# Optimization experiments

Hardware: AMD Instinct MI355X
Metric: run time of the kernel (lower is better)

The kernel has to match this reference:

```python
import jax, jax.numpy as jnp
import numpy as np

FEAT_STRIDE = 16
SCALES = (4, 8, 16, 32)
RATIOS = (0.5, 1.0, 2.0)
A = len(SCALES) * len(RATIOS)  # 12 anchors per location
PRE_NMS = 6000
POST_NMS = 300
NMS_THRESH = 0.7
MIN_SIZE = 16.0
B, C_IN, HF, WF = 4, 768, 64, 64


def _generate_anchors():
    base = np.array([0.0, 0.0, 15.0, 15.0])

    def whctrs(a):
        w = a[2] - a[0] + 1.0
        h = a[3] - a[1] + 1.0
        return w, h, a[0] + 0.5 * (w - 1.0), a[1] + 0.5 * (h - 1.0)

    def mk(ws, hs, xc, yc):
        ws = np.asarray(ws, dtype=np.float64)[:, None]
        hs = np.asarray(hs, dtype=np.float64)[:, None]
        return np.hstack([xc - 0.5 * (ws - 1), yc - 0.5 * (hs - 1),
                          xc + 0.5 * (ws - 1), yc + 0.5 * (hs - 1)])

    w, h, xc, yc = whctrs(base)
    size = w * h
    ratios = np.array(RATIOS)
    ws = np.round(np.sqrt(size / ratios))
    hs = np.round(ws * ratios)
    ratio_anchors = mk(ws, hs, xc, yc)
    scales = np.array(SCALES, dtype=np.float64)
    out = []
    for i in range(ratio_anchors.shape[0]):
        w, h, xc, yc = whctrs(ratio_anchors[i])
        out.append(mk(w * scales, h * scales, xc, yc))
    return np.vstack(out).astype(np.float32)  # (A, 4)


def _all_anchors(hf, wf):
    an = _generate_anchors()
    sx = np.arange(wf) * FEAT_STRIDE
    sy = np.arange(hf) * FEAT_STRIDE
    sx, sy = np.meshgrid(sx, sy)
    shifts = np.stack([sx.ravel(), sy.ravel(), sx.ravel(), sy.ravel()], axis=1).astype(np.float32)
    # shift-major, anchor-minor: (K, A, 4) -> (K*A, 4) matches bbox_pred layout
    return jnp.asarray((shifts[:, None, :] + an[None, :, :]).reshape(-1, 4))


def _conv(x, w, b):
    y = jax.lax.conv_general_dilated(x, w, (1, 1), 'SAME',
                                     dimension_numbers=('NCHW', 'OIHW', 'NCHW'))
    return y + b[None, :, None, None]


def _decode(anchors, deltas):
    w = anchors[:, 2] - anchors[:, 0] + 1.0
    h = anchors[:, 3] - anchors[:, 1] + 1.0
    cx = anchors[:, 0] + 0.5 * w
    cy = anchors[:, 1] + 0.5 * h
    dx, dy, dw, dh = deltas[:, 0], deltas[:, 1], deltas[:, 2], deltas[:, 3]
    pcx = dx * w + cx
    pcy = dy * h + cy
    pw = jnp.exp(dw) * w
    ph = jnp.exp(dh) * h
    return jnp.stack([pcx - 0.5 * pw, pcy - 0.5 * ph,
                      pcx + 0.5 * pw, pcy + 0.5 * ph], axis=1)


def _nms_keep(boxes, thresh):
    # greedy NMS on score-sorted boxes; returns boolean keep mask
    boxes = jax.lax.stop_gradient(boxes)
    n = boxes.shape[0]
    x1, y1, x2, y2 = boxes[:, 0], boxes[:, 1], boxes[:, 2], boxes[:, 3]
    areas = (x2 - x1 + 1.0) * (y2 - y1 + 1.0)
    idx = jnp.arange(n)

    def body(keep, i):
        xx1 = jnp.maximum(x1[i], x1)
        yy1 = jnp.maximum(y1[i], y1)
        xx2 = jnp.minimum(x2[i], x2)
        yy2 = jnp.minimum(y2[i], y2)
        inter = jnp.maximum(xx2 - xx1 + 1.0, 0.0) * jnp.maximum(yy2 - yy1 + 1.0, 0.0)
        iou = inter / (areas[i] + areas - inter)
        suppress = (iou > thresh) & (idx > i) & keep[i]
        return keep & ~suppress, None

    keep, _ = jax.lax.scan(body, jnp.ones(n, dtype=bool), jnp.arange(n))
    return keep


def _proposal_single(scores, deltas, anchors, im_info):
    # scores: (N,), deltas: (N,4), im_info: (3,) = [h, w, scale]
    boxes = _decode(anchors, deltas)
    x1 = jnp.clip(boxes[:, 0], 0.0, im_info[1] - 1.0)
    y1 = jnp.clip(boxes[:, 1], 0.0, im_info[0] - 1.0)
    x2 = jnp.clip(boxes[:, 2], 0.0, im_info[1] - 1.0)
    y2 = jnp.clip(boxes[:, 3], 0.0, im_info[0] - 1.0)
    boxes = jnp.stack([x1, y1, x2, y2], axis=1)
    ms = MIN_SIZE * im_info[2]
    valid = ((x2 - x1 + 1.0) >= ms) & ((y2 - y1 + 1.0) >= ms)
    scores = jnp.where(valid, scores, -jnp.inf)
    _, top_idx = jax.lax.top_k(scores, PRE_NMS)
    boxes = boxes[top_idx]
    keep = _nms_keep(boxes, NMS_THRESH)
    # first POST_NMS kept indices (boxes already score-sorted); zero-pad shortfall
    sel = jnp.sort(jnp.where(keep, jnp.arange(PRE_NMS), PRE_NMS))[:POST_NMS]
    pad = sel == PRE_NMS
    sel = jnp.minimum(sel, PRE_NMS - 1)
    return boxes[sel] * (~pad)[:, None].astype(boxes.dtype)


def setup_inputs() -> dict:
    key = jax.random.key(0)
    ks = jax.random.split(key, 4)
    features = jax.random.normal(ks[0], (B, C_IN, HF, WF), dtype=jnp.float32)
    im_info = jnp.tile(jnp.array([[1024.0, 1024.0, 1.0]], dtype=jnp.float32), (B, 1))
    W1 = jax.random.normal(ks[1], (512, C_IN, 3, 3), dtype=jnp.float32) * (2.0 / (C_IN * 9)) ** 0.5
    b1 = jnp.zeros((512,), dtype=jnp.float32)
    Ws = jax.random.normal(ks[2], (2 * A, 512, 1, 1), dtype=jnp.float32) * 0.01
    bs = jnp.zeros((2 * A,), dtype=jnp.float32)
    Wb = jax.random.normal(ks[3], (4 * A, 512, 1, 1), dtype=jnp.float32) * 0.01
    bb = jnp.zeros((4 * A,), dtype=jnp.float32)
    return {"features": features, "im_info": im_info, "W1": W1, "b1": b1,
            "Ws": Ws, "bs": bs, "Wb": Wb, "bb": bb}


def reference(features, im_info, W1, b1, Ws, bs, Wb, bb):
    # RPN head: 3x3 conv + relu, then 1x1 score/bbox heads
    x = jax.nn.relu(_conv(features, W1, b1))
    cls = _conv(x, Ws, bs)       # (B, 2A, H, W)
    bbox = _conv(x, Wb, bb)      # (B, 4A, H, W)
    b, _, hf, wf = cls.shape
    # view(B, 2, -1, W) softmax over class dim, view back -> channels [0:A]=bg, [A:2A]=fg
    prob = jax.nn.softmax(cls.reshape(b, 2, -1, wf), axis=1).reshape(cls.shape)
    fg = prob[:, A:, :, :]
    scores = fg.transpose(0, 2, 3, 1).reshape(b, -1)          # (B, H*W*A)
    deltas = bbox.transpose(0, 2, 3, 1).reshape(b, -1, 4)     # (B, H*W*A, 4)
    anchors = _all_anchors(hf, wf)
    boxes = jax.vmap(lambda s, d, ii: _proposal_single(s, d, anchors, ii))(scores, deltas, im_info)
    batch_idx = jnp.repeat(jnp.arange(b, dtype=boxes.dtype), POST_NMS)[:, None]
    rois = jnp.concatenate([batch_idx, boxes.reshape(-1, 4)], axis=1)  # (B*POST_NMS, 5)
    return rois
```

## Files before the change

kernel.cpp:

```cpp
#include <hip/hip_runtime.h>
#include <stdint.h>

#define CIN 768
#define CMID 512
#define NPIX 4096
#define NANCH 49152
#define NBATCH 4
#define PRE_NMS_N 6000
#define POST_NMS_N 300

__global__ void zeroK(uint32_t* __restrict__ p, int nWords){
  int i = blockIdx.x * 256 + threadIdx.x;
  if (i < nWords) p[i] = 0u;
}

__global__ __launch_bounds__(256) void conv3x3K(
    const float* __restrict__ feat, const float* __restrict__ W1,
    const float* __restrict__ b1, float* __restrict__ xout){
  __shared__ float wLds[9216];
  __shared__ float fLds[960];
  const int tid = threadIdx.x;
  const int g  = tid >> 3;
  const int py = tid & 7;
  const int ty0 = (blockIdx.x >> 3) << 3;
  const int tx0 = (blockIdx.x & 7) << 3;
  const int ocb = blockIdx.y << 7;
  const int b = blockIdx.z;

  const int oc_t  = tid >> 1;
  const int halfw = tid & 1;
  const float* wsrc0 = W1 + (size_t)(ocb + oc_t)*6912 + halfw*36;
  const int gq   = (oc_t>>2)*12 + (oc_t&3)*3;
  const int icl0 = halfw << 2;

  int fdst[4]; int fsrc[4]; bool fgo[4]; bool fact[4];
#pragma unroll
  for (int i=0;i<4;i++){
    int lin = tid + (i<<8);
    fact[i] = lin < 800;
    int l2 = fact[i] ? lin : 0;
    int ic = l2/100; int r2 = l2 - ic*100;
    int row = r2/10; int col = r2 - row*10;
    int gy = ty0 + row - 1, gx = tx0 + col - 1;
    fgo[i]  = fact[i] && gy>=0 && gy<64 && gx>=0 && gx<64;
    fdst[i] = ic*120 + row*12 + col;
    fsrc[i] = (ic<<12) + (gy<<6) + gx;
  }
  const float* fbase = feat + ((size_t)(b*CIN) << 12);

  float macc[4][8];
  float cacc[4][8];
#pragma unroll
  for (int q=0;q<4;q++)
#pragma unroll
    for (int j=0;j<8;j++){ macc[q][j]=0.0f; cacc[q][j]=0.0f; }

  for (int icb = 0; icb < CIN; icb += 8){
    {
      const float* s = wsrc0 + (size_t)icb*9;
      float w0[36];
#pragma unroll
      for (int m=0;m<9;m++){
        float4 v = *reinterpret_cast<const float4*>(s + (m<<2));
        w0[4*m+0]=v.x; w0[4*m+1]=v.y; w0[4*m+2]=v.z; w0[4*m+3]=v.w;
      }
#pragma unroll
      for (int r=0;r<4;r++)
#pragma unroll
        for (int k=0;k<9;k++)
          wLds[(icl0+r)*1152 + (k/3)*384 + gq + (k%3)] = w0[r*9+k];
    }
#pragma unroll
    for (int i=0;i<4;i++){
      if (fact[i]){
        float v = 0.0f;
        if (fgo[i]) v = fbase[((size_t)icb << 12) + fsrc[i]];
        fLds[fdst[i]] = v;
      }
    }
    __syncthreads();
#pragma unroll
    for (int ic=0; ic<8; ic++){
      const float* fb = &fLds[ic*120 + py*12];
      const float* wb = &wLds[ic*1152 + g*12];
#pragma unroll
      for (int ky=0;ky<3;ky++){
        float4 a = *reinterpret_cast<const float4*>(fb + ky*12);
        float4 c = *reinterpret_cast<const float4*>(fb + ky*12 + 4);
        float2 e = *reinterpret_cast<const float2*>(fb + ky*12 + 8);
        const float f[10] = {a.x,a.y,a.z,a.w,c.x,c.y,c.z,c.w,e.x,e.y};
        const float* wp = wb + ky*384;
        float4 wa = *reinterpret_cast<const float4*>(wp);
        float4 wv = *reinterpret_cast<const float4*>(wp+4);
        float4 wc = *reinterpret_cast<const float4*>(wp+8);
        const float w12[12] = {wa.x,wa.y,wa.z,wa.w, wv.x,wv.y,wv.z,wv.w,
                               wc.x,wc.y,wc.z,wc.w};
#pragma unroll
        for (int q=0;q<4;q++)
#pragma unroll
          for (int kx=0;kx<3;kx++){
            float we = w12[q*3+kx];
#pragma unroll
            for (int j=0;j<8;j++)
              cacc[q][j] = fmaf(we, f[j+kx], cacc[q][j]);
          }
      }
      if ((ic & 3) == 3){
#pragma unroll
        for (int q=0;q<4;q++)
#pragma unroll
          for (int j=0;j<8;j++){
            macc[q][j] = __fadd_rn(macc[q][j], cacc[q][j]);
            cacc[q][j] = 0.0f;
          }
      }
    }
    __syncthreads();
  }
#pragma unroll
  for (int q=0;q<4;q++){
    float bias = b1[ocb + (g<<2) + q];
    float4 o0, o1;
    float* p0 = (float*)&o0; float* p1 = (float*)&o1;
#pragma unroll
    for (int j=0;j<4;j++){
      p0[j] = fmaxf(__fadd_rn(macc[q][j],   bias), 0.0f);
      p1[j] = fmaxf(__fadd_rn(macc[q][j+4], bias), 0.0f);
    }
    size_t base = ((size_t)(b*CMID + ocb + (g<<2) + q) << 12) + ((ty0+py) << 6) + tx0;
    *reinterpret_cast<float4*>(&xout[base])     = o0;
    *reinterpret_cast<float4*>(&xout[base + 4]) = o1;
  }
}

__global__ __launch_bounds__(256) void conv1x1K(
    const float* __restrict__ x,
    const float* __restrict__ Ws, const float* __restrict__ bs,
    const float* __restrict__ Wb, const float* __restrict__ bb,
    float* __restrict__ clsRaw, float* __restrict__ bboxRaw){
  __shared__ float wLds[32*72];
  const int tid = threadIdx.x;
  const int px = tid & 63;
  const int og = tid >> 6;
  const int px0 = (blockIdx.x & 63) << 6;
  const int b = blockIdx.x >> 6;
  double m[18];
  float cc[18];
#pragma unroll
  for (int j=0;j<18;j++){ m[j]=0.0; cc[j]=0.0f; }
  for (int cb=0; cb<CMID; cb+=32){
#pragma unroll
    for (int i=0;i<9;i++){
      int lin = tid + i*256;
      int c = lin / 72;
      int j = lin - c*72;
      wLds[lin] = (j < 24) ? Ws[(size_t)j*512 + cb + c]
                           : Wb[(size_t)(j-24)*512 + cb + c];
    }
    __syncthreads();
    for (int c=0;c<32;c++){
      float xv = x[((size_t)(b*CMID + cb + c) << 12) + px0 + px];
      const float* wp = &wLds[c*72 + og*18];
#pragma unroll
      for (int j=0;j<18;j++) cc[j] = fmaf(wp[j], xv, cc[j]);
    }
#pragma unroll
    for (int j=0;j<18;j++){ m[j] += (double)cc[j]; cc[j]=0.0f; }
    __syncthreads();
  }
#pragma unroll
  for (int j=0;j<18;j++){
    int jg = og*18 + j;
    float bias = (jg < 24) ? bs[jg] : bb[jg-24];
    float v = __fadd_rn((float)m[j], bias);
    if (jg < 24) clsRaw[((size_t)(b*24 + jg) << 12) + px0 + px] = v;
    else         bboxRaw[((size_t)(b*48 + jg - 24) << 12) + px0 + px] = v;
  }
}

__global__ void decodeK(const float* __restrict__ clsRaw,
                        const float* __restrict__ bboxRaw,
                        const float* __restrict__ imInfo,
                        float* __restrict__ boxes, uint32_t* __restrict__ ubits,
                        uint32_t* __restrict__ hist1){
  int n = blockIdx.x*256 + threadIdx.x;
  if (n >= NBATCH*NANCH) return;
  int b = n / NANCH;
  int r = n - b*NANCH;
  int px = r / 12;
  int a = r - px*12;
  int yi = px >> 6, xi = px & 63;
  const int w0t[3] = {23,16,11};
  const int h0t[3] = {12,16,22};
  int ridx = a >> 2;
  int sh = 2 + (a & 3);
  float W = (float)(w0t[ridx] << sh);
  float H = (float)(h0t[ridx] << sh);
  float cx = (float)((xi << 4) + 8);
  float cy = (float)((yi << 4) + 8);

  size_t cbase = ((size_t)b*24 << 12) + px;
  float sc0 = clsRaw[cbase + ((size_t)a       << 12)];
  float sc1 = clsRaw[cbase + ((size_t)(12+a)  << 12)];
  size_t bbase = ((size_t)b*48 << 12) + px;
  float dx = bboxRaw[bbase + ((size_t)(4*a+0) << 12)];
  float dy = bboxRaw[bbase + ((size_t)(4*a+1) << 12)];
  float dw = bboxRaw[bbase + ((size_t)(4*a+2) << 12)];
  float dh = bboxRaw[bbase + ((size_t)(4*a+3) << 12)];

  float imh = imInfo[b*3+0], imw = imInfo[b*3+1], iscale = imInfo[b*3+2];

  float pcx = __fadd_rn(__fmul_rn(dx, W), cx);
  float pcy = __fadd_rn(__fmul_rn(dy, H), cy);
  float pw  = __fmul_rn(expf(dw), W);
  float ph  = __fmul_rn(expf(dh), H);
  float hw = __fmul_rn(0.5f, pw), hh = __fmul_rn(0.5f, ph);
  float x1 = __fsub_rn(pcx, hw), x2 = __fadd_rn(pcx, hw);
  float y1 = __fsub_rn(pcy, hh), y2 = __fadd_rn(pcy, hh);
  float xmax = __fsub_rn(imw, 1.0f), ymax = __fsub_rn(imh, 1.0f);
  x1 = fminf(fmaxf(x1, 0.0f), xmax);
  y1 = fminf(fmaxf(y1, 0.0f), ymax);
  x2 = fminf(fmaxf(x2, 0.0f), xmax);
  y2 = fminf(fmaxf(y2, 0.0f), ymax);
  float ms = __fmul_rn(16.0f, iscale);
  bool valid = (__fadd_rn(__fsub_rn(x2,x1),1.0f) >= ms) &&
               (__fadd_rn(__fsub_rn(y2,y1),1.0f) >= ms);

  float mm = fmaxf(sc0, sc1);
  float e0 = expf(__fsub_rn(sc0, mm));
  float e1 = expf(__fsub_rn(sc1, mm));
  float s  = __fdiv_rn(e1, __fadd_rn(e0, e1));

  uint32_t u = __float_as_uint(s);
  u = (u & 0x80000000u) ? ~u : (u | 0x80000000u);
  if (!valid) u = 0x007FFFFFu;

  float4 bx = make_float4(x1, y1, x2, y2);
  *reinterpret_cast<float4*>(&boxes[(size_t)n*4]) = bx;
  ubits[n] = u;
  atomicAdd(&hist1[((size_t)b << 16) + (u >> 16)], 1u);
}

__global__ void histLoK(const uint32_t* __restrict__ ubits,
                        const uint32_t* __restrict__ thrWS, uint32_t* __restrict__ hist2){
  int n = blockIdx.x*256 + threadIdx.x;
  if (n >= NBATCH*NANCH) return;
  int b = n / NANCH;
  uint32_t u = ubits[n];
  if ((u >> 16) == thrWS[b*4+0])
    atomicAdd(&hist2[((size_t)b << 16) + (u & 0xFFFFu)], 1u);
}

__global__ __launch_bounds__(1024) void selectK(const uint32_t* __restrict__ hist,
                                                uint32_t* __restrict__ thrWS, int stage){
  __shared__ uint32_t sA[1024];
  const int b = blockIdx.x;
  const uint32_t* h = hist + ((size_t)b << 16);
  const int tid = threadIdx.x;
  uint32_t base = (stage == 0) ? 0u : thrWS[b*4+1];
  uint32_t seg = 0;
  int b0 = tid << 6;
  for (int k=0;k<64;k++) seg += h[b0+k];
  sA[tid] = seg;
  __syncthreads();
  for (int off=1; off<1024; off<<=1){
    uint32_t v = (tid+off < 1024) ? sA[tid+off] : 0u;
    __syncthreads();
    sA[tid] += v;
    __syncthreads();
  }
  uint32_t inc = sA[tid];
  uint32_t above = inc - seg;
  if (base + above < 6000u && base + inc >= 6000u){
    uint32_t c = base + above;
    for (int bin = b0+63; bin >= b0; bin--){
      uint32_t hh = h[bin];
      if (c + hh >= 6000u){
        if (stage == 0){ thrWS[b*4+0] = (uint32_t)bin; thrWS[b*4+1] = c; }
        else { thrWS[b*4+2] = (thrWS[b*4+0] << 16) | (uint32_t)bin; thrWS[b*4+3] = c; }
        break;
      }
      c += hh;
    }
  }
}

__global__ void compactK(const uint32_t* __restrict__ ubits,
                         const uint32_t* __restrict__ thrWS,
                         uint32_t* __restrict__ cnts,
                         uint64_t* __restrict__ keyHi, uint64_t* __restrict__ keyEq){
  int n = blockIdx.x*256 + threadIdx.x;
  if (n >= NBATCH*NANCH) return;
  int b = n / NANCH;
  int r = n - b*NANCH;
  uint32_t u = ubits[n];
  uint32_t us = thrWS[b*4+2];
  if (u < us) return;
  uint64_t key = ((uint64_t)(~u) << 32) | (uint32_t)r;
  if (u > us){
    uint32_t p = atomicAdd(&cnts[b*2+0], 1u);
    if (p < 8192u) keyHi[((size_t)b << 13) + p] = key;
  } else {
    uint32_t p = atomicAdd(&cnts[b*2+1], 1u);
    if (p < 8192u) keyEq[((size_t)b << 13) + p] = key;
  }
}

__global__ __launch_bounds__(1024) void sortGatherK(
    const uint64_t* __restrict__ keyHi, const uint64_t* __restrict__ keyEq,
    const uint32_t* __restrict__ cnts, const float* __restrict__ boxes,
    float* __restrict__ rbox){
  __shared__ uint64_t keys[8192];
  const int b = blockIdx.x;
  const int tid = threadIdx.x;
  uint32_t nHi = cnts[b*2+0];
  if (nHi > 8192u) nHi = 8192u;
  uint32_t nEq = cnts[b*2+1];
  if (nEq > 8192u - nHi) nEq = 8192u - nHi;
  for (int i=tid; i<8192; i+=1024){
    uint64_t k;
    if (i < (int)nHi) k = keyHi[((size_t)b << 13) + i];
    else if (i < (int)(nHi + nEq)) k = keyEq[((size_t)b << 13) + (i - nHi)];
    else k = ~0ULL;
    keys[i] = k;
  }
  __syncthreads();
  for (unsigned kk = 2; kk <= 8192; kk <<= 1){
    for (unsigned j = kk >> 1; j > 0; j >>= 1){
      for (unsigned i = tid; i < 8192; i += 1024){
        unsigned l = i ^ j;
        if (l > i){
          bool up = ((i & kk) == 0);
          uint64_t a = keys[i], c = keys[l];
          if ((a > c) == up){ keys[i] = c; keys[l] = a; }
        }
      }
      __syncthreads();
    }
  }
  for (int r = tid; r < PRE_NMS_N; r += 1024){
    uint32_t idx = (uint32_t)(keys[r] & 0xFFFFFFFFu);
    float4 v = *reinterpret_cast<const float4*>(&boxes[((size_t)b*NANCH + idx)*4]);
    *reinterpret_cast<float4*>(&rbox[((size_t)b*PRE_NMS_N + r)*4]) = v;
  }
}

__global__ __launch_bounds__(64) void nmsMaskK(const float* __restrict__ rbox,
                                               uint64_t* __restrict__ mask){
  const int b = blockIdx.z;
  const int ib = blockIdx.y;
  const int jb = blockIdx.x;
  const int lane = threadIdx.x;
  uint64_t* mrow = &mask[(size_t)b*PRE_NMS_N*96];
  if (jb < ib){
    int ig = (ib << 6) + lane;
    if (ig < PRE_NMS_N) mrow[(size_t)ig*96 + jb] = 0ull;
    return;
  }
  __shared__ float rb[64][4];
  const int ig0 = ib << 6;
  {
    int ig = ig0 + lane;
    float4 v = make_float4(0.f,0.f,0.f,0.f);
    if (ig < PRE_NMS_N) v = *reinterpret_cast<const float4*>(&rbox[((size_t)b*PRE_NMS_N + ig)*4]);
    rb[lane][0]=v.x; rb[lane][1]=v.y; rb[lane][2]=v.z; rb[lane][3]=v.w;
  }
  const int jg = (jb << 6) + lane;
  const bool jok = jg < PRE_NMS_N;
  float4 cb = make_float4(0.f,0.f,0.f,0.f);
  if (jok) cb = *reinterpret_cast<const float4*>(&rbox[((size_t)b*PRE_NMS_N + jg)*4]);
  float areaJ = __fmul_rn(__fadd_rn(__fsub_rn(cb.z,cb.x),1.0f),
                          __fadd_rn(__fsub_rn(cb.w,cb.y),1.0f));
  __syncthreads();
#pragma unroll 4
  for (int i=0;i<64;i++){
    int ig = ig0 + i;
    if (ig >= PRE_NMS_N) break;
    float x1=rb[i][0], y1=rb[i][1], x2=rb[i][2], y2=rb[i][3];
    float areaI = __fmul_rn(__fadd_rn(__fsub_rn(x2,x1),1.0f),
                            __fadd_rn(__fsub_rn(y2,y1),1.0f));
    float xx1 = fmaxf(x1, cb.x);
    float yy1 = fmaxf(y1, cb.y);
    float xx2 = fminf(x2, cb.z);
    float yy2 = fminf(y2, cb.w);
    float ww = fmaxf(__fadd_rn(__fsub_rn(xx2,xx1),1.0f), 0.0f);
    float hh = fmaxf(__fadd_rn(__fsub_rn(yy2,yy1),1.0f), 0.0f);
    float inter = __fmul_rn(ww,hh);
    float iou = __fdiv_rn(inter, __fsub_rn(__fadd_rn(areaI, areaJ), inter));
    bool bit = jok && (jg > ig) && (iou > 0.7f);
    uint64_t wword = __ballot(bit);
    if (lane == 0) mrow[(size_t)ig*96 + jb] = wword;
  }
}

__global__ __launch_bounds__(64) void nmsScanK(const float* __restrict__ rbox,
                                               const uint64_t* __restrict__ mask,
                                               float* __restrict__ out){
  const int b = blockIdx.x;
  const int lane = threadIdx.x;
  const uint64_t* mrow = &mask[(size_t)b*PRE_NMS_N*96];
  uint64_t s0 = 0ull, s1 = 0ull;
  int cnt = 0;
  for (int i=0; i<PRE_NMS_N; i++){
    int w = i >> 6;
    uint64_t sw = (w < 64) ? __shfl(s0, w) : __shfl(s1, w-64);
    if (!((sw >> (i & 63)) & 1ull)){
      if (lane == 0){
        const float* s = &rbox[((size_t)b*PRE_NMS_N + i)*4];
        float* o = &out[(size_t)(b*POST_NMS_N + cnt)*5];
        o[0] = (float)b; o[1]=s[0]; o[2]=s[1]; o[3]=s[2]; o[4]=s[3];
      }
      cnt++;
      if (cnt == POST_NMS_N) break;
      const uint64_t* mr = mrow + (size_t)i*96;
      s0 |= mr[lane];
      if (lane < 30) s1 |= mr[64+lane];
    }
  }
  for (int r = cnt + lane; r < POST_NMS_N; r += 64){
    float* o = &out[(size_t)(b*POST_NMS_N + r)*5];
    o[0] = (float)b; o[1]=0.f; o[2]=0.f; o[3]=0.f; o[4]=0.f;
  }
}

extern "C" void kernel_launch(void* const* d_in, const int* in_sizes, int n_in,
                              void* d_out, int out_size, void* d_ws, size_t ws_size,
                              hipStream_t stream) {
  const float* features = (const float*)d_in[0];
  const float* im_info  = (const float*)d_in[1];
  const float* W1 = (const float*)d_in[2];
  const float* b1 = (const float*)d_in[3];
  const float* Ws = (const float*)d_in[4];
  const float* bs = (const float*)d_in[5];
  const float* Wb = (const float*)d_in[6];
  const float* bb = (const float*)d_in[7];
  float* out = (float*)d_out;
  char* ws = (char*)d_ws;

  const size_t offX     = 0;
  const size_t offCls   = offX     + (size_t)4*512*4096*4;
  const size_t offBbox  = offCls   + (size_t)4*24*4096*4;
  const size_t offBoxes = offBbox  + (size_t)4*48*4096*4;
  const size_t offU     = offBoxes + (size_t)4*49152*4*4;
  const size_t offH1    = offU     + (size_t)4*49152*4;
  const size_t offH2    = offH1    + (size_t)4*65536*4;
  const size_t offCtr   = offH2    + (size_t)4*65536*4;
  const size_t offKHi   = offCtr   + 256;
  const size_t offKEq   = offKHi   + (size_t)4*8192*8;
  const size_t offRbox  = offKEq   + (size_t)4*8192*8;

  float*    x       = (float*)(ws + offX);
  float*    clsRaw  = (float*)(ws + offCls);
  float*    bboxRaw = (float*)(ws + offBbox);
  float*    boxes   = (float*)(ws + offBoxes);
  uint32_t* ubits   = (uint32_t*)(ws + offU);
  uint32_t* hist1   = (uint32_t*)(ws + offH1);
  uint32_t* hist2   = (uint32_t*)(ws + offH2);
  uint32_t* thrWS   = (uint32_t*)(ws + offCtr);
  uint32_t* cnts    = thrWS + 16;
  uint64_t* keyHi   = (uint64_t*)(ws + offKHi);
  uint64_t* keyEq   = (uint64_t*)(ws + offKEq);
  float*    rbox    = (float*)(ws + offRbox);
  uint64_t* mask    = (uint64_t*)(ws + offX);

  {
    int nWords = (int)(((offCtr + 256) - offH1) / 4);
    int grid = (nWords + 255) / 256;
    zeroK<<<grid, 256, 0, stream>>>((uint32_t*)(ws + offH1), nWords);
  }
  conv3x3K<<<dim3(64, 4, 4), 256, 0, stream>>>(features, W1, b1, x);
  conv1x1K<<<256, 256, 0, stream>>>(x, Ws, bs, Wb, bb, clsRaw, bboxRaw);
  {
    int grid = (NBATCH*NANCH + 255) / 256;
    decodeK<<<grid, 256, 0, stream>>>(clsRaw, bboxRaw, im_info, boxes, ubits, hist1);
    selectK<<<4, 1024, 0, stream>>>(hist1, thrWS, 0);
    histLoK<<<grid, 256, 0, stream>>>(ubits, thrWS, hist2);
    selectK<<<4, 1024, 0, stream>>>(hist2, thrWS, 1);
    compactK<<<grid, 256, 0, stream>>>(ubits, thrWS, cnts, keyHi, keyEq);
  }
  sortGatherK<<<4, 1024, 0, stream>>>(keyHi, keyEq, cnts, boxes, rbox);
  nmsMaskK<<<dim3(94, 94, 4), 64, 0, stream>>>(rbox, mask);
  nmsScanK<<<4, 64, 0, stream>>>(rbox, mask, out);
}
```

Measured before the change: 2.498 ms.

## Widen conv3x3 tile to 8x16 pixels and use packed FP32 FMA

The 3x3 conv tile grows from 8x8 to 8x16 output pixels per block, which halves the grid and doubles each thread's work to 16 pixels times 4 output channels. Weights staged in LDS are now reused across twice as many pixels. The inner accumulation uses two-wide float vectors so the compiler can emit packed FMA instructions, which process two FP32 values per instruction on CDNA3/4. The cost is higher register pressure and a larger LDS feature tile, with only 512 blocks left for occupancy.

```diff
diff --git a/kernel.cpp b/kernel.cpp
--- a/kernel.cpp
+++ b/kernel.cpp
@@ -9,6 +9,20 @@
 #define PRE_NMS_N 6000
 #define POST_NMS_N 300
 
+typedef float v2f __attribute__((ext_vector_type(2)));
+
+#if defined(__has_builtin)
+#if __has_builtin(__builtin_elementwise_fma)
+#define PKFMA(a,b,c) __builtin_elementwise_fma(a,b,c)
+#endif
+#endif
+#ifndef PKFMA
+static __device__ inline v2f pkfma_fallback(v2f a, v2f b, v2f c){
+  v2f r; r.x = fmaf(a.x,b.x,c.x); r.y = fmaf(a.y,b.y,c.y); return r;
+}
+#define PKFMA(a,b,c) pkfma_fallback(a,b,c)
+#endif
+
 __global__ void zeroK(uint32_t* __restrict__ p, int nWords){
   int i = blockIdx.x * 256 + threadIdx.x;
   if (i < nWords) p[i] = 0u;
@@ -18,12 +32,12 @@
     const float* __restrict__ feat, const float* __restrict__ W1,
     const float* __restrict__ b1, float* __restrict__ xout){
   __shared__ float wLds[9216];
-  __shared__ float fLds[960];
+  __shared__ float fLds[4864];
   const int tid = threadIdx.x;
   const int g  = tid >> 3;
   const int py = tid & 7;
-  const int ty0 = (blockIdx.x >> 3) << 3;
-  const int tx0 = (blockIdx.x & 7) << 3;
+  const int ty0 = (blockIdx.x >> 2) << 3;
+  const int tx0 = (blockIdx.x & 3) << 4;
   const int ocb = blockIdx.y << 7;
   const int b = blockIdx.z;
 
@@ -33,27 +47,27 @@
   const int gq   = (oc_t>>2)*12 + (oc_t&3)*3;
   const int icl0 = halfw << 2;
 
-  int fdst[4]; int fsrc[4]; bool fgo[4]; bool fact[4];
-#pragma unroll
-  for (int i=0;i<4;i++){
+  int fdst[6]; int fsrc[6]; bool fgo[6]; bool fact[6];
+#pragma unroll
+  for (int i=0;i<6;i++){
     int lin = tid + (i<<8);
-    fact[i] = lin < 800;
+    fact[i] = lin < 1440;
     int l2 = fact[i] ? lin : 0;
-    int ic = l2/100; int r2 = l2 - ic*100;
-    int row = r2/10; int col = r2 - row*10;
+    int ic = l2/180; int r2 = l2 - ic*180;
+    int row = r2/18; int col = r2 - row*18;
     int gy = ty0 + row - 1, gx = tx0 + col - 1;
     fgo[i]  = fact[i] && gy>=0 && gy<64 && gx>=0 && gx<64;
-    fdst[i] = ic*120 + row*12 + col;
+    fdst[i] = ic*200 + row*20 + col;
     fsrc[i] = (ic<<12) + (gy<<6) + gx;
   }
   const float* fbase = feat + ((size_t)(b*CIN) << 12);
 
-  float macc[4][8];
-  float cacc[4][8];
+  v2f macc[4][8];
+  v2f cacc[4][8];
 #pragma unroll
   for (int q=0;q<4;q++)
 #pragma unroll
-    for (int j=0;j<8;j++){ macc[q][j]=0.0f; cacc[q][j]=0.0f; }
+    for (int j2=0;j2<8;j2++){ macc[q][j2] = (v2f){0.f,0.f}; cacc[q][j2] = (v2f){0.f,0.f}; }
 
   for (int icb = 0; icb < CIN; icb += 8){
     {
@@ -71,7 +85,7 @@
           wLds[(icl0+r)*1152 + (k/3)*384 + gq + (k%3)] = w0[r*9+k];
     }
 #pragma unroll
-    for (int i=0;i<4;i++){
+    for (int i=0;i<6;i++){
       if (fact[i]){
         float v = 0.0f;
         if (fgo[i]) v = fbase[((size_t)icb << 12) + fsrc[i]];
@@ -81,37 +95,49 @@
     __syncthreads();
 #pragma unroll
     for (int ic=0; ic<8; ic++){
-      const float* fb = &fLds[ic*120 + py*12];
+      const float* fb = &fLds[ic*200 + py*20];
       const float* wb = &wLds[ic*1152 + g*12];
 #pragma unroll
       for (int ky=0;ky<3;ky++){
-        float4 a = *reinterpret_cast<const float4*>(fb + ky*12);
-        float4 c = *reinterpret_cast<const float4*>(fb + ky*12 + 4);
-        float2 e = *reinterpret_cast<const float2*>(fb + ky*12 + 8);
-        const float f[10] = {a.x,a.y,a.z,a.w,c.x,c.y,c.z,c.w,e.x,e.y};
+        const float* fp = fb + ky*20;
+        float4 A  = *reinterpret_cast<const float4*>(fp);
+        float4 Bv = *reinterpret_cast<const float4*>(fp+4);
+        float4 C  = *reinterpret_cast<const float4*>(fp+8);
+        float4 D  = *reinterpret_cast<const float4*>(fp+12);
+        float2 E  = *reinterpret_cast<const float2*>(fp+16);
+        const float f[18] = {A.x,A.y,A.z,A.w, Bv.x,Bv.y,Bv.z,Bv.w,
+                             C.x,C.y,C.z,C.w, D.x,D.y,D.z,D.w, E.x,E.y};
         const float* wp = wb + ky*384;
-        float4 wa = *reinterpret_cast<const float4*>(wp);
-        float4 wv = *reinterpret_cast<const float4*>(wp+4);
-        float4 wc = *reinterpret_cast<const float4*>(wp+8);
-        const float w12[12] = {wa.x,wa.y,wa.z,wa.w, wv.x,wv.y,wv.z,wv.w,
+        float4 wa  = *reinterpret_cast<const float4*>(wp);
+        float4 wm  = *reinterpret_cast<const float4*>(wp+4);
+        float4 wc  = *reinterpret_cast<const float4*>(wp+8);
+        const float w12[12] = {wa.x,wa.y,wa.z,wa.w, wm.x,wm.y,wm.z,wm.w,
                                wc.x,wc.y,wc.z,wc.w};
+        v2f P[3][8];
+#pragma unroll
+        for (int j2=0;j2<8;j2++){
+          P[0][j2] = (v2f){f[2*j2],   f[2*j2+1]};
+          P[1][j2] = (v2f){f[2*j2+1], f[2*j2+2]};
+          P[2][j2] = (v2f){f[2*j2+2], f[2*j2+3]};
+        }
 #pragma unroll
         for (int q=0;q<4;q++)
 #pragma unroll
           for (int kx=0;kx<3;kx++){
             float we = w12[q*3+kx];
-#pragma unroll
-            for (int j=0;j<8;j++)
-              cacc[q][j] = fmaf(we, f[j+kx], cacc[q][j]);
+            v2f wv = (v2f){we, we};
+#pragma unroll
+            for (int j2=0;j2<8;j2++)
+              cacc[q][j2] = PKFMA(wv, P[kx][j2], cacc[q][j2]);
           }
       }
       if ((ic & 3) == 3){
 #pragma unroll
         for (int q=0;q<4;q++)
 #pragma unroll
-          for (int j=0;j<8;j++){
-            macc[q][j] = __fadd_rn(macc[q][j], cacc[q][j]);
-            cacc[q][j] = 0.0f;
+          for (int j2=0;j2<8;j2++){
+            macc[q][j2] = macc[q][j2] + cacc[q][j2];
+            cacc[q][j2] = (v2f){0.f,0.f};
           }
       }
     }
@@ -120,16 +146,19 @@
 #pragma unroll
   for (int q=0;q<4;q++){
     float bias = b1[ocb + (g<<2) + q];
-    float4 o0, o1;
-    float* p0 = (float*)&o0; float* p1 = (float*)&o1;
-#pragma unroll
-    for (int j=0;j<4;j++){
-      p0[j] = fmaxf(__fadd_rn(macc[q][j],   bias), 0.0f);
-      p1[j] = fmaxf(__fadd_rn(macc[q][j+4], bias), 0.0f);
+    float o[16];
+#pragma unroll
+    for (int j2=0;j2<8;j2++){
+      o[2*j2]   = fmaxf(__fadd_rn(macc[q][j2].x, bias), 0.0f);
+      o[2*j2+1] = fmaxf(__fadd_rn(macc[q][j2].y, bias), 0.0f);
     }
     size_t base = ((size_t)(b*CMID + ocb + (g<<2) + q) << 12) + ((ty0+py) << 6) + tx0;
-    *reinterpret_cast<float4*>(&xout[base])     = o0;
-    *reinterpret_cast<float4*>(&xout[base + 4]) = o1;
+#pragma unroll
+    for (int m=0;m<4;m++){
+      float4 ov; float* p = (float*)&ov;
+      p[0]=o[4*m]; p[1]=o[4*m+1]; p[2]=o[4*m+2]; p[3]=o[4*m+3];
+      *reinterpret_cast<float4*>(&xout[base + 4*m]) = ov;
+    }
   }
 }
 
@@ -468,7 +497,7 @@
     int grid = (nWords + 255) / 256;
     zeroK<<<grid, 256, 0, stream>>>((uint32_t*)(ws + offH1), nWords);
   }
-  conv3x3K<<<dim3(64, 4, 4), 256, 0, stream>>>(features, W1, b1, x);
+  conv3x3K<<<dim3(32, 4, 4), 256, 0, stream>>>(features, W1, b1, x);
   conv1x1K<<<256, 256, 0, stream>>>(x, Ws, bs, Wb, bb, clsRaw, bboxRaw);
   {
     int grid = (NBATCH*NANCH + 255) / 256;
```

Result: slower. 5.479 ms (+119.4%).
